# Kernel tuning notes

Measured on AMD Instinct MI355X. Metric: run time of the kernel, lower is better.

The kernel has to match this reference:

```python
import jax, jax.numpy as jnp
import numpy as np

B, S, D, H = 2, 2048, 2048, 16
DK = D // H


def setup_inputs() -> dict:
    key = jax.random.key(0)
    k1, k2, k3 = jax.random.split(key, 3)
    x = jax.random.normal(k1, (B, S, D), dtype=jnp.float32)
    # trunc-normal in the original; plain normal with matching std is fine for a numeric baseline
    std_qkv = 2.0 / (DK + D)  # note: original passes variance as std to trunc_normal_
    W_qkv = jax.random.normal(k2, (3 * D, D), dtype=jnp.float32) * std_qkv
    W_o = jax.random.normal(k3, (D, D), dtype=jnp.float32) * (1.0 / D)
    return {"x": x, "W_qkv": W_qkv, "W_o": W_o}


def reference(x, W_qkv, W_o):
    b, s, d = x.shape
    # fused QKV projection: y = x @ W_qkv^T
    qkv = jnp.einsum('bsd,ed->bse', x, W_qkv)  # [b, s, 3d]
    q, k, v = jnp.split(qkv, 3, axis=-1)
    # [b, s, d] -> [b, h, s, dk]
    def to_heads(t):
        return t.reshape(b, s, H, DK).transpose(0, 2, 1, 3)
    q, k, v = to_heads(q), to_heads(k), to_heads(v)
    scores = jnp.einsum('bhqd,bhkd->bhqk', q, k) / np.sqrt(DK).astype(np.float32)
    causal = jnp.tril(jnp.ones((s, s), dtype=bool))
    scores = jnp.where(causal, scores, -jnp.inf)
    att = jax.nn.softmax(scores, axis=-1)
    out = jnp.einsum('bhqk,bhkd->bhqd', att, v)  # [b, h, s, dk]
    out = out.transpose(0, 2, 1, 3).reshape(b, s, d)
    return jnp.einsum('bsd,od->bso', out, W_o)
```

## Files before the change

kernel.cpp:

```cpp
#include <hip/hip_runtime.h>

typedef _Float16 f16;
typedef _Float16 f16x4 __attribute__((ext_vector_type(4)));
typedef _Float16 f16x8 __attribute__((ext_vector_type(8)));
typedef float    f32x4 __attribute__((ext_vector_type(4)));

#define MFMA_F16(a,b,c) __builtin_amdgcn_mfma_f32_16x16x32_f16((a),(b),(c),0,0,0)

static constexpr int B_  = 2;
static constexpr int S_  = 2048;
static constexpr int D_  = 2048;
static constexpr int H_  = 16;
static constexpr int DK_ = 128;
static constexpr int K_  = 2048;
static constexpr int NKT = 64;

__device__ __forceinline__ void gload_lds16(const void* g, void* l) {
  __builtin_amdgcn_global_load_lds(
      (const __attribute__((address_space(1))) void*)g,
      (__attribute__((address_space(3))) void*)l, 16, 0, 0);
}

__global__ __launch_bounds__(256) void cast_f16_kernel(const float* __restrict__ in,
                                                       f16* __restrict__ out, int n4) {
  int i = blockIdx.x * 256 + threadIdx.x;
  int stride = gridDim.x * 256;
  for (int j = i; j < n4; j += stride) {
    float4 v = reinterpret_cast<const float4*>(in)[j];
    f16x4 o = {(f16)v.x, (f16)v.y, (f16)v.z, (f16)v.w};
    reinterpret_cast<f16x4*>(out)[j] = o;
  }
}


__device__ __forceinline__ void ring_stage3(const f16* gA, const f16* gB, int t,
                                            char* slot, int w) {
  gload_lds16(gA + (size_t)(w * 16) * K_ + t * 32,        slot + w * 1024);
  gload_lds16(gA + (size_t)((w + 4) * 16) * K_ + t * 32,  slot + (w + 4) * 1024);
  gload_lds16(gB + (size_t)(w * 16) * K_ + t * 32,        slot + 8192 + w * 1024);
  gload_lds16(gB + (size_t)((w + 4) * 16) * K_ + t * 32,  slot + 8192 + (w + 4) * 1024);
}

__device__ __forceinline__ void ring_step3(const char* slot, int wr, int wc, int lro,
                                           f32x4 (&acc)[4][4]) {
  f16x8 af[4], bf[4];
#pragma unroll
  for (int mi = 0; mi < 4; ++mi)
    af[mi] = *(const f16x8*)(slot + (wr * 4 + mi) * 1024 + lro);
#pragma unroll
  for (int ni = 0; ni < 4; ++ni)
    bf[ni] = *(const f16x8*)(slot + 8192 + (wc * 4 + ni) * 1024 + lro);
  __builtin_amdgcn_s_setprio(1);
#pragma unroll
  for (int mi = 0; mi < 4; ++mi)
#pragma unroll
    for (int ni = 0; ni < 4; ++ni)
      acc[mi][ni] = MFMA_F16(af[mi], bf[ni], acc[mi][ni]);
  __builtin_amdgcn_s_setprio(0);
}

#define SYNC3(N)                                              \
  asm volatile("s_waitcnt vmcnt(" #N ")" ::: "memory");       \
  __builtin_amdgcn_s_barrier();                               \
  asm volatile("" ::: "memory");

#define STEP3(CS, TT, SS)                                     \
  ring_stage3(gA, gB, (TT), (SS), w);                         \
  ring_step3((CS), wr, wc, lro, acc);                         \
  SYNC3(4)

__device__ __forceinline__ void gemm_core3(const f16* __restrict__ A,
                                           const f16* __restrict__ Bw,
                                           int brow, int bcol, char* lds,
                                           f32x4 (&acc)[4][4]) {
  const int tid = threadIdx.x;
  const int w = tid >> 6, l = tid & 63;
  const int lg = l >> 4, lr = l & 15;
  const int wr = w >> 1, wc = w & 1;
  const int lro = (lr * 4 + (lg ^ ((lr >> 1) & 3))) * 16;

#pragma unroll
  for (int mi = 0; mi < 4; ++mi)
#pragma unroll
    for (int ni = 0; ni < 4; ++ni) acc[mi][ni] = (f32x4){0.f, 0.f, 0.f, 0.f};

  const int kgsrc = (l & 3) ^ ((l >> 3) & 3);
  const f16* gA = A  + (size_t)(brow * 128 + (l >> 2)) * K_ + kgsrc * 8;
  const f16* gB = Bw + (size_t)(bcol * 128 + (l >> 2)) * K_ + kgsrc * 8;

  char* s0 = lds;
  char* s1 = lds + 16384;
  char* s2 = lds + 32768;

  ring_stage3(gA, gB, 0, s0, w);
  ring_stage3(gA, gB, 1, s1, w);
  SYNC3(4)

  for (int tb = 0; tb < 20; ++tb) {
    const int t = 3 * tb;
    STEP3(s0, t + 2, s2)
    STEP3(s1, t + 3, s0)
    STEP3(s2, t + 4, s1)
  }
  STEP3(s0, 62, s2)
  STEP3(s1, 63, s0)
  ring_step3(s2, wr, wc, lro, acc);
  asm volatile("s_waitcnt vmcnt(0)" ::: "memory");
  __builtin_amdgcn_s_barrier();
  asm volatile("" ::: "memory");
  ring_step3(s0, wr, wc, lro, acc);
}

__global__ __launch_bounds__(256, 3) void gemm_qkv_kernel(const f16* __restrict__ xb,
                                                          const f16* __restrict__ wqkv,
                                                          f16* __restrict__ Q,
                                                          f16* __restrict__ Kk,
                                                          f16* __restrict__ Vt) {
  __shared__ __align__(16) char lds[49152];
  const int bid = blockIdx.x;
  const int xcd = bid & 7;
  const int local = bid >> 3;
  const int brow = (xcd >> 1) * 8 + (local & 7);
  const int bcol = (xcd & 1) * 24 + (local >> 3);

  f32x4 acc[4][4];
  gemm_core3(xb, wqkv, brow, bcol, lds, acc);

  const int tid = threadIdx.x;
  const int w = tid >> 6, l = tid & 63;
  const int lg = l >> 4, lr = l & 15;
  const int wr = w >> 1, wc = w & 1;

  const int which = bcol / 16;
  const int h = bcol % 16;

  if (which == 2) {
#pragma unroll
    for (int mi = 0; mi < 4; ++mi) {
      const int mbase = brow * 128 + wr * 64 + mi * 16 + lg * 4;
      const int b = mbase >> 11, s = mbase & 2047;
#pragma unroll
      for (int ni = 0; ni < 4; ++ni) {
        const int dk = wc * 64 + ni * 16 + lr;
        f16x4 v = {(f16)acc[mi][ni][0], (f16)acc[mi][ni][1],
                   (f16)acc[mi][ni][2], (f16)acc[mi][ni][3]};
        *(f16x4*)(Vt + ((size_t)(b * H_ + h) * DK_ + dk) * S_ + s) = v;
      }
    }
  } else {
    f16* outp = (which == 0) ? Q : Kk;
    const float scale = (which == 0) ? 0.08838834764831845f : 1.0f;
#pragma unroll
    for (int mi = 0; mi < 4; ++mi) {
      const int mbase = brow * 128 + wr * 64 + mi * 16 + lg * 4;
#pragma unroll
      for (int ni = 0; ni < 4; ++ni) {
        const int dk = wc * 64 + ni * 16 + lr;
#pragma unroll
        for (int r = 0; r < 4; ++r) {
          const int mm = mbase + r;
          const int b = mm >> 11, s = mm & 2047;
          outp[(((size_t)b * H_ + h) * S_ + s) * DK_ + dk] = (f16)(acc[mi][ni][r] * scale);
        }
      }
    }
  }
}

__global__ __launch_bounds__(256, 3) void gemm_out_kernel(const f16* __restrict__ ab,
                                                          const f16* __restrict__ wo,
                                                          float* __restrict__ out) {
  __shared__ __align__(16) char lds[49152];
  const int bid = blockIdx.x;
  const int xcd = bid & 7;
  const int local = bid >> 3;
  const int brow = (xcd >> 1) * 8 + (local & 7);
  const int bcol = (xcd & 1) * 8 + (local >> 3);

  f32x4 acc[4][4];
  gemm_core3(ab, wo, brow, bcol, lds, acc);

  const int tid = threadIdx.x;
  const int w = tid >> 6, l = tid & 63;
  const int lg = l >> 4, lr = l & 15;
  const int wr = w >> 1, wc = w & 1;

#pragma unroll
  for (int mi = 0; mi < 4; ++mi) {
    const int mbase = brow * 128 + wr * 64 + mi * 16 + lg * 4;
#pragma unroll
    for (int ni = 0; ni < 4; ++ni) {
      const int n = bcol * 128 + wc * 64 + ni * 16 + lr;
#pragma unroll
      for (int r = 0; r < 4; ++r)
        out[(size_t)(mbase + r) * D_ + n] = acc[mi][ni][r];
    }
  }
}

__global__ __launch_bounds__(256) void attn_kernel(const f16* __restrict__ Q,
                                                   const f16* __restrict__ Kg,
                                                   const f16* __restrict__ Vt,
                                                   f16* __restrict__ O) {
  __shared__ __align__(16) unsigned char Ks[64 * 256];
  __shared__ __align__(16) unsigned char Vs[128 * 128];
  __shared__ __align__(16) unsigned char Ps[4][16 * 128];

  const int bid = blockIdx.x;
  const int pr = bid & 15;
  const int h  = (bid >> 4) & 15;
  const int b  = bid >> 8;
  const int bh = b * H_ + h;
  const int tid = threadIdx.x;
  const int w = tid >> 6, l = tid & 63;
  const int lg = l >> 4, lr = l & 15;

  for (int half = 0; half < 2; ++half) {
    const int qt = half ? (31 - pr) : pr;

    const f16* Qg = Q + ((size_t)bh * S_ + qt * 64 + w * 16) * DK_;
    f16x8 qf[4];
#pragma unroll
    for (int kd = 0; kd < 4; ++kd)
      qf[kd] = *(const f16x8*)(Qg + (size_t)lr * DK_ + kd * 32 + lg * 8);

    f32x4 o[8];
#pragma unroll
    for (int n = 0; n < 8; ++n) o[n] = (f32x4){0.f, 0.f, 0.f, 0.f};
    float mrun[4] = {-1e30f, -1e30f, -1e30f, -1e30f};
    float lrun[4] = {0.f, 0.f, 0.f, 0.f};

    const int ntiles = qt + 1;
    for (int kt = 0; kt < ntiles; ++kt) {
      __syncthreads();
      const f16* Kt = Kg + ((size_t)bh * S_ + kt * 64) * DK_;
#pragma unroll
      for (int i = 0; i < 4; ++i) {
        const int chunk = i * 256 + tid;
        const int row = chunk >> 4, c8 = chunk & 15;
        uint4 v = *(const uint4*)(Kt + (size_t)row * DK_ + c8 * 8);
        *(uint4*)(Ks + row * 256 + ((c8 * 16) ^ ((row & 7) << 4))) = v;
      }
      const f16* Vtt = Vt + (size_t)bh * DK_ * S_ + kt * 64;
#pragma unroll
      for (int i = 0; i < 4; ++i) {
        const int chunk = i * 256 + tid;
        const int row = chunk >> 3, c8 = chunk & 7;
        uint4 v = *(const uint4*)(Vtt + (size_t)row * S_ + c8 * 8);
        *(uint4*)(Vs + row * 128 + ((c8 * 16) ^ ((row & 7) << 4))) = v;
      }
      __syncthreads();

      f32x4 s[4];
#pragma unroll
      for (int j = 0; j < 4; ++j) s[j] = (f32x4){0.f, 0.f, 0.f, 0.f};
      __builtin_amdgcn_s_setprio(1);
#pragma unroll
      for (int j = 0; j < 4; ++j) {
        const int row = j * 16 + lr;
#pragma unroll
        for (int kd = 0; kd < 4; ++kd) {
          f16x8 kf = *(const f16x8*)(Ks + row * 256 + ((kd * 64 + lg * 16) ^ ((row & 7) << 4)));
          s[j] = MFMA_F16(qf[kd], kf, s[j]);
        }
      }
      __builtin_amdgcn_s_setprio(0);
      if (kt == qt) {
#pragma unroll
        for (int j = 0; j < 4; ++j) {
          const int col = j * 16 + lr;
#pragma unroll
          for (int r = 0; r < 4; ++r) {
            const int qrow = w * 16 + lg * 4 + r;
            if (col > qrow) s[j][r] = -1e30f;
          }
        }
      }
      float scl[4];
#pragma unroll
      for (int r = 0; r < 4; ++r) {
        float m0 = fmaxf(fmaxf(s[0][r], s[1][r]), fmaxf(s[2][r], s[3][r]));
#pragma unroll
        for (int msk = 1; msk < 16; msk <<= 1) m0 = fmaxf(m0, __shfl_xor(m0, msk, 64));
        const float nm = fmaxf(mrun[r], m0);
        scl[r] = __expf(mrun[r] - nm);
        mrun[r] = nm;
      }
      float rs[4] = {0.f, 0.f, 0.f, 0.f};
#pragma unroll
      for (int j = 0; j < 4; ++j) {
#pragma unroll
        for (int r = 0; r < 4; ++r) {
          const float p = __expf(fmaxf(s[j][r] - mrun[r], -80.f));
          rs[r] += p;
          const int row = lg * 4 + r;
          const int cb = (j * 16 + lr) * 2;
          *(f16*)(Ps[w] + row * 128 + (cb ^ ((row & 7) << 4))) = (f16)p;
        }
      }
#pragma unroll
      for (int r = 0; r < 4; ++r) {
        float t = rs[r];
#pragma unroll
        for (int msk = 1; msk < 16; msk <<= 1) t += __shfl_xor(t, msk, 64);
        lrun[r] = lrun[r] * scl[r] + t;
      }
#pragma unroll
      for (int n = 0; n < 8; ++n)
#pragma unroll
        for (int r = 0; r < 4; ++r) o[n][r] *= scl[r];

      asm volatile("s_waitcnt lgkmcnt(0)" ::: "memory");

      __builtin_amdgcn_s_setprio(1);
#pragma unroll
      for (int ks = 0; ks < 2; ++ks) {
        f16x8 pf = *(const f16x8*)(Ps[w] + lr * 128 + ((ks * 64 + lg * 16) ^ ((lr & 7) << 4)));
#pragma unroll
        for (int n = 0; n < 8; ++n) {
          const int row = n * 16 + lr;
          f16x8 vf = *(const f16x8*)(Vs + row * 128 + ((ks * 64 + lg * 16) ^ ((row & 7) << 4)));
          o[n] = MFMA_F16(pf, vf, o[n]);
        }
      }
      __builtin_amdgcn_s_setprio(0);
    }

#pragma unroll
    for (int r = 0; r < 4; ++r) {
      const float inv = 1.0f / lrun[r];
      const int srow = qt * 64 + w * 16 + lg * 4 + r;
      f16* op = O + ((size_t)b * S_ + srow) * D_ + h * DK_;
#pragma unroll
      for (int n = 0; n < 8; ++n) op[n * 16 + lr] = (f16)(o[n][r] * inv);
    }
  }
}

extern "C" void kernel_launch(void* const* d_in, const int* in_sizes, int n_in,
                              void* d_out, int out_size, void* d_ws, size_t ws_size,
                              hipStream_t stream) {
  const float* x    = (const float*)d_in[0];
  const float* wqkv = (const float*)d_in[1];
  const float* wo   = (const float*)d_in[2];
  float* out = (float*)d_out;
  char* ws = (char*)d_ws;

  f16* xb     = (f16*)(ws + 0);
  f16* wqkvb  = (f16*)(ws + 16777216);
  f16* wob    = (f16*)(ws + 41943040);
  f16* Qb     = (f16*)(ws + 50331648);
  f16* Kb     = (f16*)(ws + 67108864);
  f16* Vtb    = (f16*)(ws + 83886080);
  f16* attn_o = (f16*)(ws + 0);

  cast_f16_kernel<<<2048, 256, 0, stream>>>(x, xb, 8388608 / 4);
  cast_f16_kernel<<<2048, 256, 0, stream>>>(wqkv, wqkvb, 12582912 / 4);
  cast_f16_kernel<<<1024, 256, 0, stream>>>(wo, wob, 4194304 / 4);

  gemm_qkv_kernel<<<1536, 256, 0, stream>>>(xb, wqkvb, Qb, Kb, Vtb);
  attn_kernel<<<512, 256, 0, stream>>>(Qb, Kb, Vtb, attn_o);
  gemm_out_kernel<<<512, 256, 0, stream>>>(attn_o, wob, out);
}
```

Baseline: 287.4 us.

## Widen GEMM tiles to 128x256 with 8 waves and a 4-stage LDS ring

Both projection GEMMs now use 512-thread blocks computing 128x256 output tiles, with eight waves arranged 2x4, each still producing a 64x64 sub-tile. The K pipeline moves from a 3-slot to a 4-slot LDS ring of 24 KB slots (96 KB total), keeping three stages in flight. Wider tiles cut repeated A-operand global loads and the grid shrinks accordingly. In exchange, LDS use per block rises sharply, fewer blocks fit per CU, and the output GEMM launches only 256 blocks, which risks underfilling the GPU.

```diff
diff --git a/kernel.cpp b/kernel.cpp
--- a/kernel.cpp
+++ b/kernel.cpp
@@ -13,7 +13,6 @@
 static constexpr int H_  = 16;
 static constexpr int DK_ = 128;
 static constexpr int K_  = 2048;
-static constexpr int NKT = 64;
 
 __device__ __forceinline__ void gload_lds16(const void* g, void* l) {
   __builtin_amdgcn_global_load_lds(
@@ -33,23 +32,22 @@
 }
 
 
-__device__ __forceinline__ void ring_stage3(const f16* gA, const f16* gB, int t,
-                                            char* slot, int w) {
-  gload_lds16(gA + (size_t)(w * 16) * K_ + t * 32,        slot + w * 1024);
-  gload_lds16(gA + (size_t)((w + 4) * 16) * K_ + t * 32,  slot + (w + 4) * 1024);
-  gload_lds16(gB + (size_t)(w * 16) * K_ + t * 32,        slot + 8192 + w * 1024);
-  gload_lds16(gB + (size_t)((w + 4) * 16) * K_ + t * 32,  slot + 8192 + (w + 4) * 1024);
-}
-
-__device__ __forceinline__ void ring_step3(const char* slot, int wr, int wc, int lro,
-                                           f32x4 (&acc)[4][4]) {
+__device__ __forceinline__ void stage_ph(const f16* gA, const f16* gB, int t,
+                                         char* slot, int w) {
+  gload_lds16(gA + (size_t)(w * 16) * K_ + t * 32,       slot + w * 1024);
+  gload_lds16(gB + (size_t)(w * 16) * K_ + t * 32,       slot + 8192 + w * 1024);
+  gload_lds16(gB + (size_t)((w + 8) * 16) * K_ + t * 32, slot + 8192 + (w + 8) * 1024);
+}
+
+__device__ __forceinline__ void mfma_ph(const char* slot, int aoff, int boff, int lro,
+                                        f32x4 (&acc)[4][4]) {
   f16x8 af[4], bf[4];
 #pragma unroll
   for (int mi = 0; mi < 4; ++mi)
-    af[mi] = *(const f16x8*)(slot + (wr * 4 + mi) * 1024 + lro);
+    af[mi] = *(const f16x8*)(slot + aoff + mi * 1024 + lro);
 #pragma unroll
   for (int ni = 0; ni < 4; ++ni)
-    bf[ni] = *(const f16x8*)(slot + 8192 + (wc * 4 + ni) * 1024 + lro);
+    bf[ni] = *(const f16x8*)(slot + boff + ni * 1024 + lro);
   __builtin_amdgcn_s_setprio(1);
 #pragma unroll
   for (int mi = 0; mi < 4; ++mi)
@@ -59,25 +57,22 @@
   __builtin_amdgcn_s_setprio(0);
 }
 
-#define SYNC3(N)                                              \
+#define SYNCW(N)                                              \
   asm volatile("s_waitcnt vmcnt(" #N ")" ::: "memory");       \
   __builtin_amdgcn_s_barrier();                               \
   asm volatile("" ::: "memory");
 
-#define STEP3(CS, TT, SS)                                     \
-  ring_stage3(gA, gB, (TT), (SS), w);                         \
-  ring_step3((CS), wr, wc, lro, acc);                         \
-  SYNC3(4)
-
-__device__ __forceinline__ void gemm_core3(const f16* __restrict__ A,
-                                           const f16* __restrict__ Bw,
-                                           int brow, int bcol, char* lds,
-                                           f32x4 (&acc)[4][4]) {
+__device__ __forceinline__ void gemm_core_w8(const f16* __restrict__ A,
+                                             const f16* __restrict__ Bw,
+                                             int brow, int bcol, char* lds,
+                                             f32x4 (&acc)[4][4]) {
   const int tid = threadIdx.x;
   const int w = tid >> 6, l = tid & 63;
   const int lg = l >> 4, lr = l & 15;
-  const int wr = w >> 1, wc = w & 1;
+  const int wm = w >> 2, wn = w & 3;
   const int lro = (lr * 4 + (lg ^ ((lr >> 1) & 3))) * 16;
+  const int aoff = wm * 4096;
+  const int boff = 8192 + wn * 4096;
 
 #pragma unroll
   for (int mi = 0; mi < 4; ++mi)
@@ -86,62 +81,63 @@
 
   const int kgsrc = (l & 3) ^ ((l >> 3) & 3);
   const f16* gA = A  + (size_t)(brow * 128 + (l >> 2)) * K_ + kgsrc * 8;
-  const f16* gB = Bw + (size_t)(bcol * 128 + (l >> 2)) * K_ + kgsrc * 8;
+  const f16* gB = Bw + (size_t)(bcol * 256 + (l >> 2)) * K_ + kgsrc * 8;
 
   char* s0 = lds;
-  char* s1 = lds + 16384;
-  char* s2 = lds + 32768;
-
-  ring_stage3(gA, gB, 0, s0, w);
-  ring_stage3(gA, gB, 1, s1, w);
-  SYNC3(4)
-
-  for (int tb = 0; tb < 20; ++tb) {
-    const int t = 3 * tb;
-    STEP3(s0, t + 2, s2)
-    STEP3(s1, t + 3, s0)
-    STEP3(s2, t + 4, s1)
-  }
-  STEP3(s0, 62, s2)
-  STEP3(s1, 63, s0)
-  ring_step3(s2, wr, wc, lro, acc);
-  asm volatile("s_waitcnt vmcnt(0)" ::: "memory");
-  __builtin_amdgcn_s_barrier();
-  asm volatile("" ::: "memory");
-  ring_step3(s0, wr, wc, lro, acc);
-}
-
-__global__ __launch_bounds__(256, 3) void gemm_qkv_kernel(const f16* __restrict__ xb,
-                                                          const f16* __restrict__ wqkv,
-                                                          f16* __restrict__ Q,
-                                                          f16* __restrict__ Kk,
-                                                          f16* __restrict__ Vt) {
-  __shared__ __align__(16) char lds[49152];
+  char* s1 = lds + 24576;
+  char* s2 = lds + 49152;
+  char* s3 = lds + 73728;
+
+  stage_ph(gA, gB, 0, s0, w);
+  stage_ph(gA, gB, 1, s1, w);
+  stage_ph(gA, gB, 2, s2, w);
+  SYNCW(6)
+
+  for (int tb = 0; tb < 15; ++tb) {
+    const int t = tb * 4;
+    stage_ph(gA, gB, t + 3, s3, w); mfma_ph(s0, aoff, boff, lro, acc); SYNCW(6)
+    stage_ph(gA, gB, t + 4, s0, w); mfma_ph(s1, aoff, boff, lro, acc); SYNCW(6)
+    stage_ph(gA, gB, t + 5, s1, w); mfma_ph(s2, aoff, boff, lro, acc); SYNCW(6)
+    stage_ph(gA, gB, t + 6, s2, w); mfma_ph(s3, aoff, boff, lro, acc); SYNCW(6)
+  }
+  stage_ph(gA, gB, 63, s3, w); mfma_ph(s0, aoff, boff, lro, acc); SYNCW(6)
+  mfma_ph(s1, aoff, boff, lro, acc); SYNCW(3)
+  mfma_ph(s2, aoff, boff, lro, acc); SYNCW(0)
+  mfma_ph(s3, aoff, boff, lro, acc);
+}
+
+__global__ __launch_bounds__(512) void gemm_qkv_kernel(const f16* __restrict__ xb,
+                                                       const f16* __restrict__ wqkv,
+                                                       f16* __restrict__ Q,
+                                                       f16* __restrict__ Kk,
+                                                       f16* __restrict__ Vt) {
+  __shared__ __align__(16) char lds[98304];
   const int bid = blockIdx.x;
   const int xcd = bid & 7;
   const int local = bid >> 3;
-  const int brow = (xcd >> 1) * 8 + (local & 7);
-  const int bcol = (xcd & 1) * 24 + (local >> 3);
+  const int brow = xcd * 4 + (local & 3);
+  const int bcol = local >> 2;
 
   f32x4 acc[4][4];
-  gemm_core3(xb, wqkv, brow, bcol, lds, acc);
+  gemm_core_w8(xb, wqkv, brow, bcol, lds, acc);
 
   const int tid = threadIdx.x;
   const int w = tid >> 6, l = tid & 63;
   const int lg = l >> 4, lr = l & 15;
-  const int wr = w >> 1, wc = w & 1;
-
-  const int which = bcol / 16;
-  const int h = bcol % 16;
+  const int wm = w >> 2, wn = w & 3;
+
+  const int which = bcol >> 3;
+  const int nsec = (bcol & 7) * 256;
 
   if (which == 2) {
 #pragma unroll
     for (int mi = 0; mi < 4; ++mi) {
-      const int mbase = brow * 128 + wr * 64 + mi * 16 + lg * 4;
-      const int b = mbase >> 11, s = mbase & 2047;
+      const int m0 = brow * 128 + wm * 64 + mi * 16 + lg * 4;
+      const int b = m0 >> 11, s = m0 & 2047;
 #pragma unroll
       for (int ni = 0; ni < 4; ++ni) {
-        const int dk = wc * 64 + ni * 16 + lr;
+        const int n = nsec + wn * 64 + ni * 16 + lr;
+        const int h = n >> 7, dk = n & 127;
         f16x4 v = {(f16)acc[mi][ni][0], (f16)acc[mi][ni][1],
                    (f16)acc[mi][ni][2], (f16)acc[mi][ni][3]};
         *(f16x4*)(Vt + ((size_t)(b * H_ + h) * DK_ + dk) * S_ + s) = v;
@@ -152,13 +148,14 @@
     const float scale = (which == 0) ? 0.08838834764831845f : 1.0f;
 #pragma unroll
     for (int mi = 0; mi < 4; ++mi) {
-      const int mbase = brow * 128 + wr * 64 + mi * 16 + lg * 4;
+      const int m0 = brow * 128 + wm * 64 + mi * 16 + lg * 4;
 #pragma unroll
       for (int ni = 0; ni < 4; ++ni) {
-        const int dk = wc * 64 + ni * 16 + lr;
+        const int n = nsec + wn * 64 + ni * 16 + lr;
+        const int h = n >> 7, dk = n & 127;
 #pragma unroll
         for (int r = 0; r < 4; ++r) {
-          const int mm = mbase + r;
+          const int mm = m0 + r;
           const int b = mm >> 11, s = mm & 2047;
           outp[(((size_t)b * H_ + h) * S_ + s) * DK_ + dk] = (f16)(acc[mi][ni][r] * scale);
         }
@@ -167,33 +164,33 @@
   }
 }
 
-__global__ __launch_bounds__(256, 3) void gemm_out_kernel(const f16* __restrict__ ab,
-                                                          const f16* __restrict__ wo,
-                                                          float* __restrict__ out) {
-  __shared__ __align__(16) char lds[49152];
+__global__ __launch_bounds__(512) void gemm_out_kernel(const f16* __restrict__ ab,
+                                                       const f16* __restrict__ wo,
+                                                       float* __restrict__ out) {
+  __shared__ __align__(16) char lds[98304];
   const int bid = blockIdx.x;
   const int xcd = bid & 7;
   const int local = bid >> 3;
-  const int brow = (xcd >> 1) * 8 + (local & 7);
-  const int bcol = (xcd & 1) * 8 + (local >> 3);
+  const int brow = xcd * 4 + (local & 3);
+  const int bcol = local >> 2;
 
   f32x4 acc[4][4];
-  gemm_core3(ab, wo, brow, bcol, lds, acc);
+  gemm_core_w8(ab, wo, brow, bcol, lds, acc);
 
   const int tid = threadIdx.x;
   const int w = tid >> 6, l = tid & 63;
   const int lg = l >> 4, lr = l & 15;
-  const int wr = w >> 1, wc = w & 1;
+  const int wm = w >> 2, wn = w & 3;
 
 #pragma unroll
   for (int mi = 0; mi < 4; ++mi) {
-    const int mbase = brow * 128 + wr * 64 + mi * 16 + lg * 4;
+    const int m0 = brow * 128 + wm * 64 + mi * 16 + lg * 4;
 #pragma unroll
     for (int ni = 0; ni < 4; ++ni) {
-      const int n = bcol * 128 + wc * 64 + ni * 16 + lr;
+      const int n = bcol * 256 + wn * 64 + ni * 16 + lr;
 #pragma unroll
       for (int r = 0; r < 4; ++r)
-        out[(size_t)(mbase + r) * D_ + n] = acc[mi][ni][r];
+        out[(size_t)(m0 + r) * D_ + n] = acc[mi][ni][r];
     }
   }
 }
@@ -358,7 +355,7 @@
   cast_f16_kernel<<<2048, 256, 0, stream>>>(wqkv, wqkvb, 12582912 / 4);
   cast_f16_kernel<<<1024, 256, 0, stream>>>(wo, wob, 4194304 / 4);
 
-  gemm_qkv_kernel<<<1536, 256, 0, stream>>>(xb, wqkvb, Qb, Kb, Vtb);
+  gemm_qkv_kernel<<<768, 512, 0, stream>>>(xb, wqkvb, Qb, Kb, Vtb);
   attn_kernel<<<512, 256, 0, stream>>>(Qb, Kb, Vtb, attn_o);
-  gemm_out_kernel<<<512, 256, 0, stream>>>(attn_o, wob, out);
-}
+  gemm_out_kernel<<<256, 512, 0, stream>>>(attn_o, wob, out);
+}
```

Result: faster. 269.9 us (-6.1%).
